# Kernel optimization log

Measured on AMD Instinct MI355X. Metric: run time of the kernel, lower is better.

Reference implementation:

```python
import jax, jax.numpy as jnp
import numpy as np

N_NODES = 50000
N_EDGES = 600000
IN_CH = 128
HID_CH = 128
OUT_CH = 64
DEMO = 8
N_GRAPHS = 100


def setup_inputs() -> dict:
    key = jax.random.key(0)
    ks = jax.random.split(key, 16)
    s = 0.02
    inp = {
        "x": jax.random.normal(ks[0], (N_NODES, IN_CH), jnp.float32),
        "edge_index": jax.random.randint(ks[1], (2, N_EDGES), 0, N_NODES, jnp.int32),
        "batch": jnp.sort(jax.random.randint(ks[2], (N_NODES,), 0, N_GRAPHS, jnp.int32)),
        "demographic": jax.random.normal(ks[3], (N_GRAPHS, DEMO), jnp.float32),
        "W1": jax.random.normal(ks[4], (IN_CH, HID_CH), jnp.float32) * s,
        "b1": jnp.zeros((HID_CH,), jnp.float32),
        "W2": jax.random.normal(ks[5], (HID_CH, HID_CH), jnp.float32) * s,
        "b2": jnp.zeros((HID_CH,), jnp.float32),
        "W3": jax.random.normal(ks[6], (HID_CH, OUT_CH), jnp.float32) * s,
        "b3": jnp.zeros((OUT_CH,), jnp.float32),
        "Wf1": jax.random.normal(ks[7], (OUT_CH + DEMO, 64), jnp.float32) * s,
        "bf1": jnp.zeros((64,), jnp.float32),
        "Wf2": jax.random.normal(ks[8], (64, 32), jnp.float32) * s,
        "bf2": jnp.zeros((32,), jnp.float32),
        "Wf3": jax.random.normal(ks[9], (32, 2), jnp.float32) * s,
        "bf3": jnp.zeros((2,), jnp.float32),
    }
    return inp


def _gcn_conv(x, W, b, src, dst, norm, n_nodes):
    # PyG GCNConv: out_i = sum_j norm_ij * (x_j @ W) + b  (self-loops included in src/dst)
    h = x @ W
    msg = h[src] * norm[:, None]
    return jax.ops.segment_sum(msg, dst, num_segments=n_nodes) + b


def reference(x, edge_index, batch, demographic, W1, b1, W2, b2, W3, b3, Wf1, bf1, Wf2, bf2, Wf3, bf3):
    n = x.shape[0]
    # add self-loops
    loop = jnp.arange(n, dtype=edge_index.dtype)
    src = jnp.concatenate([edge_index[0], loop])
    dst = jnp.concatenate([edge_index[1], loop])
    # symmetric degree normalization: deg^{-1/2}[src] * deg^{-1/2}[dst]
    deg = jax.ops.segment_sum(jnp.ones_like(src, jnp.float32), dst, num_segments=n)
    dinv = jnp.where(deg > 0, jax.lax.rsqrt(deg), 0.0)
    norm = dinv[src] * dinv[dst]

    h = jax.nn.relu(_gcn_conv(x, W1, b1, src, dst, norm, n))
    h = jax.nn.relu(_gcn_conv(h, W2, b2, src, dst, norm, n))
    h = jax.nn.relu(_gcn_conv(h, W3, b3, src, dst, norm, n))

    # global mean pool over graphs
    g = demographic.shape[0]
    sums = jax.ops.segment_sum(h, batch, num_segments=g)
    cnts = jax.ops.segment_sum(jnp.ones((n,), jnp.float32), batch, num_segments=g)
    pooled = sums / jnp.maximum(cnts, 1.0)[:, None]

    z = jnp.concatenate([pooled, demographic], axis=1)
    z = jax.nn.relu(z @ Wf1 + bf1)
    z = jax.nn.relu(z @ Wf2 + bf2)
    return z @ Wf3 + bf3
```

## Files before the change

kernel.cpp:

```cpp
#include <hip/hip_runtime.h>


typedef __bf16 bf16x8 __attribute__((ext_vector_type(8)));
typedef float f32x4 __attribute__((ext_vector_type(4)));
typedef float f32x2 __attribute__((ext_vector_type(2)));

__device__ __forceinline__ unsigned char f32_to_fp8(float v) {
    return (unsigned char)(__builtin_amdgcn_cvt_pk_fp8_f32(v, 0.f, 0, false) & 0xff);
}
__device__ __forceinline__ f32x2 fp8x2_to_f32(unsigned u) {
    f32x2 r = __builtin_amdgcn_cvt_pk_f32_fp8(u, false);
    return r;
}
__device__ __forceinline__ float fp8_to_f32(unsigned u) {
    f32x2 r = __builtin_amdgcn_cvt_pk_f32_fp8(u, false);
    return r.x;
}

union BF2 {
    __bf16 h[2];
    unsigned u;
};

#define PAD(c) (((c) + 15) & ~15)
#define BCAP 64
#define ECHUNK 4096

__device__ __forceinline__ void wpack_block(const float* __restrict__ W,
                                            __bf16* __restrict__ hi,
                                            __bf16* __restrict__ lo, int N, int b, int l) {
    int t = b >> 2, c = b & 3;
    int k0 = c * 32 + (l >> 4) * 8;
    int ncol = t * 16 + (l & 15);
    size_t base = ((size_t)b * 64 + l) * 8;
#pragma unroll
    for (int j = 0; j < 8; j++) {
        float v = W[(size_t)(k0 + j) * N + ncol];
        __bf16 h = (__bf16)v;
        hi[base + j] = h;
        lo[base + j] = (__bf16)(v - (float)h);
    }
}

__global__ __launch_bounds__(1024) void k_bin(const int* __restrict__ src,
                                              const int* __restrict__ dst,
                                              int2* __restrict__ binbuf,
                                              int* __restrict__ bcnt,
                                              const int* __restrict__ batch,
                                              int* __restrict__ gstart,
                                              const float* __restrict__ W1,
                                              const float* __restrict__ W2,
                                              const float* __restrict__ W3,
                                              __bf16* __restrict__ Wp1h, __bf16* __restrict__ Wp1l,
                                              __bf16* __restrict__ Wp2h, __bf16* __restrict__ Wp2l,
                                              __bf16* __restrict__ Wp3h, __bf16* __restrict__ Wp3l,
                                              int E, int EC, int nbuck, int n, int G) {
    int b = blockIdx.x;
    int tid = threadIdx.x;
    if (b < EC) {
        __shared__ int lcur[512];
        for (int i = tid; i < nbuck; i += 1024) lcur[i] = 0;
        __syncthreads();
        int e0 = b * ECHUNK;
        int cntE = E - e0;
        if (cntE > ECHUNK) cntE = ECHUNK;
#pragma unroll
        for (int k = 0; k < 4; k++) {
            int idx = tid + k * 1024;
            if (idx < cntE) {
                int s = src[e0 + idx];
                int d = dst[e0 + idx];
                int bk = d >> 7;
                int slot = atomicAdd(&lcur[bk], 1);
                if (slot < BCAP) {
                    int2 sd = {s, d};
                    binbuf[((size_t)b * nbuck + bk) * BCAP + slot] = sd;
                }
            }
        }
        __syncthreads();
        for (int bk = tid; bk < nbuck; bk += 1024) {
            int c = lcur[bk];
            bcnt[b * nbuck + bk] = (c < BCAP) ? c : BCAP;
        }
        return;
    }
    if (b == EC) {
        int g = tid;
        if (g <= G) {
            int lo = 0, hi = n;
            while (lo < hi) {
                int mid = (lo + hi) >> 1;
                if (batch[mid] < g) lo = mid + 1; else hi = mid;
            }
            gstart[g] = lo;
        }
        return;
    }
    int b64 = (b - EC - 1) * 16 + (tid >> 6);
    int l = tid & 63;
    if (b64 < 32) wpack_block(W1, Wp1h, Wp1l, 128, b64, l);
    else if (b64 < 64) wpack_block(W2, Wp2h, Wp2l, 128, b64 - 32, l);
    else if (b64 < 80) wpack_block(W3, Wp3h, Wp3l, 64, b64 - 64, l);
}

__global__ __launch_bounds__(1024) void k_rows(const int2* __restrict__ binbuf,
                                               const int* __restrict__ bcnt,
                                               int* __restrict__ gdeg,
                                               float* __restrict__ dinv,
                                               int* __restrict__ btot,
                                               unsigned int* __restrict__ tz128,
                                               unsigned int* __restrict__ tz64,
                                               int n, int EC, int nbuck) {
    __shared__ int lcnt[160];
    __shared__ int lpre[161];
    __shared__ int deg[128];
    int b = blockIdx.x;
    int tid = threadIdx.x;
    int lane = tid & 63;
    int wid = tid >> 6;
    int r0 = b << 7;
    int r1 = r0 + 128;
    if (r1 > n) r1 = n;
    int nrows = r1 - r0;
    if (b == 0) {
        if (tid < 32) tz128[(size_t)n * 32 + tid] = 0u;
        else if (tid < 48) tz64[(size_t)n * 16 + (tid - 32)] = 0u;
    }
    for (int c = tid; c < EC; c += 1024) lcnt[c] = bcnt[c * nbuck + b];
    if (tid < 128) deg[tid] = 0;
    __syncthreads();
    if (wid == 0) {
        int carry = 0;
        for (int bb = 0; bb < EC; bb += 64) {
            int idx = bb + lane;
            int val = (idx < EC) ? lcnt[idx] : 0;
            int sc = val;
#pragma unroll
            for (int d = 1; d < 64; d <<= 1) {
                int o = __shfl_up(sc, d);
                if (lane >= d) sc += o;
            }
            int grp = __shfl(sc, 63);
            if (idx < EC) lpre[idx] = sc - val + carry;
            carry += grp;
        }
        if (lane == 0) lpre[EC] = carry;
    }
    __syncthreads();
    int T = lpre[EC];
    for (int i = tid; i < T; i += 1024) {
        int lo = 0, hi = EC;
        while (lo < hi) {
            int mid = (lo + hi) >> 1;
            if (lpre[mid + 1] <= i) lo = mid + 1; else hi = mid;
        }
        int j = i - lpre[lo];
        int2 sd = binbuf[((size_t)lo * nbuck + b) * BCAP + j];
        unsigned r = (unsigned)(sd.y - r0);
        if (r < (unsigned)nrows) atomicAdd(&deg[r], 1);
    }
    __syncthreads();
    if (wid == 0) {
        int carry = 0;
#pragma unroll
        for (int bb = 0; bb < 128; bb += 64) {
            int idx = bb + lane;
            int val = (idx < nrows) ? PAD(deg[idx]) : 0;
#pragma unroll
            for (int d = 32; d > 0; d >>= 1) val += __shfl_xor(val, d);
            carry += val;
        }
        if (lane == 0) btot[b] = carry;
    }
    if (tid < nrows) {
        int d = deg[tid];
        gdeg[r0 + tid] = d;
        dinv[r0 + tid] = rsqrtf((float)(d + 1));
    }
}

__global__ __launch_bounds__(64) void k_base(const int* __restrict__ btot,
                                             int* __restrict__ bbase,
                                             int* __restrict__ rowptr,
                                             int n, int nbuck) {
    int lane = threadIdx.x;
    int carry = 0;
    for (int bb = 0; bb < nbuck; bb += 64) {
        int idx = bb + lane;
        int val = (idx < nbuck) ? btot[idx] : 0;
        int sc = val;
#pragma unroll
        for (int d = 1; d < 64; d <<= 1) {
            int o = __shfl_up(sc, d);
            if (lane >= d) sc += o;
        }
        int grp = __shfl(sc, 63);
        if (idx < nbuck) bbase[idx] = sc - val + carry;
        carry += grp;
    }
    if (lane == 0) {
        bbase[nbuck] = carry;
        rowptr[n] = carry;
    }
}

__global__ __launch_bounds__(1024) void k_place(const int2* __restrict__ binbuf,
                                                const int* __restrict__ bcnt,
                                                const int* __restrict__ gdeg,
                                                const int* __restrict__ bbase,
                                                int* __restrict__ rowptr,
                                                int* __restrict__ col,
                                                int n, int EC, int nbuck,
                                                const float* __restrict__ A,
                                                const __bf16* __restrict__ Wp_hi,
                                                const __bf16* __restrict__ Wp_lo,
                                                const float* __restrict__ dinv,
                                                unsigned char* __restrict__ Cf8) {
    int b = blockIdx.x;
    int tid = threadIdx.x;
    if (b < nbuck) {
        __shared__ int cols_s[5120];
        __shared__ int lcnt[160];
        __shared__ int lpre[161];
        __shared__ int lloc[129];
        __shared__ int lfill[128];
        int lane = tid & 63;
        int wid = tid >> 6;
        int r0 = b << 7;
        int r1 = r0 + 128;
        if (r1 > n) r1 = n;
        int nrows = r1 - r0;
        int base = bbase[b];
        int size = bbase[b + 1] - base;
        for (int c = tid; c < EC; c += 1024) lcnt[c] = bcnt[c * nbuck + b];
        __syncthreads();
        if (wid == 0) {
            int carry = 0;
            for (int bb = 0; bb < EC; bb += 64) {
                int idx = bb + lane;
                int val = (idx < EC) ? lcnt[idx] : 0;
                int sc = val;
#pragma unroll
                for (int d = 1; d < 64; d <<= 1) {
                    int o = __shfl_up(sc, d);
                    if (lane >= d) sc += o;
                }
                int grp = __shfl(sc, 63);
                if (idx < EC) lpre[idx] = sc - val + carry;
                carry += grp;
            }
            if (lane == 0) lpre[EC] = carry;
        } else if (wid == 1) {
            int carry = 0;
#pragma unroll
            for (int bb = 0; bb < 128; bb += 64) {
                int idx = bb + lane;
                int val = (idx < nrows) ? PAD(gdeg[r0 + idx]) : 0;
                int sc = val;
#pragma unroll
                for (int d = 1; d < 64; d <<= 1) {
                    int o = __shfl_up(sc, d);
                    if (lane >= d) sc += o;
                }
                int grp = __shfl(sc, 63);
                lloc[idx] = sc - val + carry;
                carry += grp;
            }
            if (lane == 0) lloc[128] = carry;
        }
        __syncthreads();
        if (tid < nrows) {
            lfill[tid] = lloc[tid];
            rowptr[r0 + tid] = base + lloc[tid];
        }
        int T = lpre[EC];
        if (size <= 5120) {
            for (int i = tid; i < size; i += 1024) cols_s[i] = n;
            __syncthreads();
            for (int i = tid; i < T; i += 1024) {
                int lo = 0, hi = EC;
                while (lo < hi) {
                    int mid = (lo + hi) >> 1;
                    if (lpre[mid + 1] <= i) lo = mid + 1; else hi = mid;
                }
                int j = i - lpre[lo];
                int2 sd = binbuf[((size_t)lo * nbuck + b) * BCAP + j];
                unsigned r = (unsigned)(sd.y - r0);
                if (r < (unsigned)nrows) {
                    int pos = atomicAdd(&lfill[r], 1);
                    if ((unsigned)pos < (unsigned)size) cols_s[pos] = sd.x;
                }
            }
            __syncthreads();
            for (int i = tid; i < size; i += 1024) col[base + i] = cols_s[i];
        } else {
            __syncthreads();
            for (int i = tid; i < T; i += 1024) {
                int lo = 0, hi = EC;
                while (lo < hi) {
                    int mid = (lo + hi) >> 1;
                    if (lpre[mid + 1] <= i) lo = mid + 1; else hi = mid;
                }
                int j = i - lpre[lo];
                int2 sd = binbuf[((size_t)lo * nbuck + b) * BCAP + j];
                unsigned r = (unsigned)(sd.y - r0);
                if (r < (unsigned)nrows) {
                    int pos = atomicAdd(&lfill[r], 1);
                    if (pos < size) col[base + pos] = sd.x;
                }
            }
            __syncthreads();
            if (tid < nrows) {
                int pend = lloc[tid + 1];
                for (int p = lloc[tid] + gdeg[r0 + tid]; p < pend; p++) col[base + p] = n;
            }
        }
        return;
    }
    constexpr int NT = 8;
    constexpr int N = NT * 16;
    int bid = b - nbuck;
    int wave = bid * 16 + (tid >> 6);
    int lane = tid & 63;
    int row0 = wave * 16;
    if (row0 >= n) return;
    int m = lane & 15;
    int q = lane >> 4;
    int row = row0 + m;
    if (row >= n) row = n - 1;
    const float* ap = A + (size_t)row * 128 + q * 8;
    bf16x8 ahi[4], alo[4];
#pragma unroll
    for (int c = 0; c < 4; c++) {
        float4 v0 = *(const float4*)(ap + c * 32);
        float4 v1 = *(const float4*)(ap + c * 32 + 4);
        float vv[8] = {v0.x, v0.y, v0.z, v0.w, v1.x, v1.y, v1.z, v1.w};
#pragma unroll
        for (int j = 0; j < 8; j++) {
            __bf16 h = (__bf16)vv[j];
            ahi[c][j] = h;
            alo[c][j] = (__bf16)(vv[j] - (float)h);
        }
    }
    float dscale[4];
#pragma unroll
    for (int r = 0; r < 4; r++) {
        int rr = row0 + q * 4 + r;
        dscale[r] = dinv[rr < n ? rr : (n - 1)];
    }
#pragma unroll
    for (int t = 0; t < NT; t++) {
        f32x4 acc = {0.f, 0.f, 0.f, 0.f};
#pragma unroll
        for (int c = 0; c < 4; c++) {
            size_t off = ((size_t)(t * 4 + c) * 64 + lane) * 8;
            bf16x8 bh = *(const bf16x8*)(Wp_hi + off);
            bf16x8 bl = *(const bf16x8*)(Wp_lo + off);
            acc = __builtin_amdgcn_mfma_f32_16x16x32_bf16(ahi[c], bh, acc, 0, 0, 0);
            acc = __builtin_amdgcn_mfma_f32_16x16x32_bf16(alo[c], bh, acc, 0, 0, 0);
            acc = __builtin_amdgcn_mfma_f32_16x16x32_bf16(ahi[c], bl, acc, 0, 0, 0);
        }
        int colx = t * 16 + m;
#pragma unroll
        for (int r = 0; r < 4; r++) {
            int orow = row0 + q * 4 + r;
            if (orow < n) Cf8[(size_t)orow * N + colx] = f32_to_fp8(acc[r] * dscale[r]);
        }
    }
}

template <int NT>
__global__ __launch_bounds__(256) void k_gemm_bf16(const __bf16* __restrict__ A,
                                                   const __bf16* __restrict__ Wp_hi,
                                                   const __bf16* __restrict__ Wp_lo,
                                                   const float* __restrict__ dinv,
                                                   unsigned char* __restrict__ Cf8, int n) {
    constexpr int N = NT * 16;
    int wave = (int)((blockIdx.x * 256u + threadIdx.x) >> 6);
    int lane = threadIdx.x & 63;
    int row0 = wave * 16;
    if (row0 >= n) return;
    int m = lane & 15;
    int q = lane >> 4;
    int row = row0 + m;
    if (row >= n) row = n - 1;
    const __bf16* ap = A + (size_t)row * 128 + q * 8;
    bf16x8 a[4];
#pragma unroll
    for (int c = 0; c < 4; c++) a[c] = *(const bf16x8*)(ap + c * 32);
    float dscale[4];
#pragma unroll
    for (int r = 0; r < 4; r++) {
        int rr = row0 + q * 4 + r;
        dscale[r] = dinv[rr < n ? rr : (n - 1)];
    }
#pragma unroll
    for (int t = 0; t < NT; t++) {
        f32x4 acc = {0.f, 0.f, 0.f, 0.f};
#pragma unroll
        for (int c = 0; c < 4; c++) {
            size_t off = ((size_t)(t * 4 + c) * 64 + lane) * 8;
            bf16x8 bh = *(const bf16x8*)(Wp_hi + off);
            bf16x8 bl = *(const bf16x8*)(Wp_lo + off);
            acc = __builtin_amdgcn_mfma_f32_16x16x32_bf16(a[c], bh, acc, 0, 0, 0);
            acc = __builtin_amdgcn_mfma_f32_16x16x32_bf16(a[c], bl, acc, 0, 0, 0);
        }
        int colx = t * 16 + m;
#pragma unroll
        for (int r = 0; r < 4; r++) {
            int orow = row0 + q * 4 + r;
            if (orow < n) Cf8[(size_t)orow * N + colx] = f32_to_fp8(acc[r] * dscale[r]);
        }
    }
}

__global__ __launch_bounds__(256) void k_agg128(const unsigned short* __restrict__ t8,
                                                const int* __restrict__ rowptr,
                                                const int* __restrict__ col,
                                                const float* __restrict__ dinv,
                                                const float* __restrict__ bias,
                                                unsigned int* __restrict__ out, int n) {
    int w = (int)((blockIdx.x * 256u + threadIdx.x) >> 6);
    int lane = threadIdx.x & 63;
    if (w >= n) return;
    f32x2 vs = fp8x2_to_f32((unsigned)t8[(size_t)w * 64 + lane]);
    float a0 = vs.x;
    float a1 = vs.y;
    int p = rowptr[w], pe = rowptr[w + 1];
    for (; p < pe; p += 16) {
        int4 c0 = *(const int4*)(col + p);
        int4 c1 = *(const int4*)(col + p + 4);
        int4 c2 = *(const int4*)(col + p + 8);
        int4 c3 = *(const int4*)(col + p + 12);
        unsigned u0 = t8[((size_t)c0.x << 6) + lane];
        unsigned u1 = t8[((size_t)c0.y << 6) + lane];
        unsigned u2 = t8[((size_t)c0.z << 6) + lane];
        unsigned u3 = t8[((size_t)c0.w << 6) + lane];
        unsigned u4 = t8[((size_t)c1.x << 6) + lane];
        unsigned u5 = t8[((size_t)c1.y << 6) + lane];
        unsigned u6 = t8[((size_t)c1.z << 6) + lane];
        unsigned u7 = t8[((size_t)c1.w << 6) + lane];
        unsigned u8 = t8[((size_t)c2.x << 6) + lane];
        unsigned u9 = t8[((size_t)c2.y << 6) + lane];
        unsigned ua = t8[((size_t)c2.z << 6) + lane];
        unsigned ub = t8[((size_t)c2.w << 6) + lane];
        unsigned uc = t8[((size_t)c3.x << 6) + lane];
        unsigned ud = t8[((size_t)c3.y << 6) + lane];
        unsigned ue = t8[((size_t)c3.z << 6) + lane];
        unsigned uf = t8[((size_t)c3.w << 6) + lane];
        f32x2 v;
        v = fp8x2_to_f32(u0); a0 += v.x; a1 += v.y;
        v = fp8x2_to_f32(u1); a0 += v.x; a1 += v.y;
        v = fp8x2_to_f32(u2); a0 += v.x; a1 += v.y;
        v = fp8x2_to_f32(u3); a0 += v.x; a1 += v.y;
        v = fp8x2_to_f32(u4); a0 += v.x; a1 += v.y;
        v = fp8x2_to_f32(u5); a0 += v.x; a1 += v.y;
        v = fp8x2_to_f32(u6); a0 += v.x; a1 += v.y;
        v = fp8x2_to_f32(u7); a0 += v.x; a1 += v.y;
        v = fp8x2_to_f32(u8); a0 += v.x; a1 += v.y;
        v = fp8x2_to_f32(u9); a0 += v.x; a1 += v.y;
        v = fp8x2_to_f32(ua); a0 += v.x; a1 += v.y;
        v = fp8x2_to_f32(ub); a0 += v.x; a1 += v.y;
        v = fp8x2_to_f32(uc); a0 += v.x; a1 += v.y;
        v = fp8x2_to_f32(ud); a0 += v.x; a1 += v.y;
        v = fp8x2_to_f32(ue); a0 += v.x; a1 += v.y;
        v = fp8x2_to_f32(uf); a0 += v.x; a1 += v.y;
    }
    float di = dinv[w];
    BF2 o;
    o.h[0] = (__bf16)fmaxf(di * a0 + bias[lane * 2], 0.f);
    o.h[1] = (__bf16)fmaxf(di * a1 + bias[lane * 2 + 1], 0.f);
    out[(size_t)w * 64 + lane] = o.u;
}

__global__ __launch_bounds__(256) void k_agg64(const unsigned char* __restrict__ t8,
                                               const int* __restrict__ rowptr,
                                               const int* __restrict__ col,
                                               const float* __restrict__ dinv,
                                               const float* __restrict__ bias,
                                               __bf16* __restrict__ out, int n) {
    int w = (int)((blockIdx.x * 256u + threadIdx.x) >> 6);
    int lane = threadIdx.x & 63;
    if (w >= n) return;
    float acc = fp8_to_f32((unsigned)t8[(size_t)w * 64 + lane]);
    int p = rowptr[w], pe = rowptr[w + 1];
    for (; p < pe; p += 16) {
        int4 c0 = *(const int4*)(col + p);
        int4 c1 = *(const int4*)(col + p + 4);
        int4 c2 = *(const int4*)(col + p + 8);
        int4 c3 = *(const int4*)(col + p + 12);
        unsigned u0 = t8[((size_t)c0.x << 6) + lane];
        unsigned u1 = t8[((size_t)c0.y << 6) + lane];
        unsigned u2 = t8[((size_t)c0.z << 6) + lane];
        unsigned u3 = t8[((size_t)c0.w << 6) + lane];
        unsigned u4 = t8[((size_t)c1.x << 6) + lane];
        unsigned u5 = t8[((size_t)c1.y << 6) + lane];
        unsigned u6 = t8[((size_t)c1.z << 6) + lane];
        unsigned u7 = t8[((size_t)c1.w << 6) + lane];
        unsigned u8 = t8[((size_t)c2.x << 6) + lane];
        unsigned u9 = t8[((size_t)c2.y << 6) + lane];
        unsigned ua = t8[((size_t)c2.z << 6) + lane];
        unsigned ub = t8[((size_t)c2.w << 6) + lane];
        unsigned uc = t8[((size_t)c3.x << 6) + lane];
        unsigned ud = t8[((size_t)c3.y << 6) + lane];
        unsigned ue = t8[((size_t)c3.z << 6) + lane];
        unsigned uf = t8[((size_t)c3.w << 6) + lane];
        acc += fp8_to_f32(u0);
        acc += fp8_to_f32(u1);
        acc += fp8_to_f32(u2);
        acc += fp8_to_f32(u3);
        acc += fp8_to_f32(u4);
        acc += fp8_to_f32(u5);
        acc += fp8_to_f32(u6);
        acc += fp8_to_f32(u7);
        acc += fp8_to_f32(u8);
        acc += fp8_to_f32(u9);
        acc += fp8_to_f32(ua);
        acc += fp8_to_f32(ub);
        acc += fp8_to_f32(uc);
        acc += fp8_to_f32(ud);
        acc += fp8_to_f32(ue);
        acc += fp8_to_f32(uf);
    }
    out[(size_t)w * 64 + lane] = (__bf16)fmaxf(dinv[w] * acc + bias[lane], 0.f);
}

__global__ __launch_bounds__(256) void k_poolmlp(const unsigned short* __restrict__ h,
                                                 const int* __restrict__ gstart,
                                                 const float* __restrict__ demo,
                                                 const float* __restrict__ Wf1,
                                                 const float* __restrict__ bf1,
                                                 const float* __restrict__ Wf2,
                                                 const float* __restrict__ bf2,
                                                 const float* __restrict__ Wf3,
                                                 const float* __restrict__ bf3,
                                                 float* __restrict__ out, int G) {
    int g = blockIdx.x;
    int tid = threadIdx.x;
    int lane = tid & 63;
    int wv = tid >> 6;
    int s = gstart[g], e = gstart[g + 1];
    float acc = 0.f;
    for (int i = s + wv; i < e; i += 4)
        acc += __uint_as_float((unsigned)h[(size_t)i * 64 + lane] << 16);
    __shared__ float red[4][64];
    __shared__ float zin[72];
    __shared__ float z1[64];
    __shared__ float z2[32];
    red[wv][lane] = acc;
    if (tid >= 64 && tid < 72) zin[tid] = demo[g * 8 + (tid - 64)];
    __syncthreads();
    if (tid < 64) {
        float v = red[0][tid] + red[1][tid] + red[2][tid] + red[3][tid];
        zin[tid] = v / fmaxf((float)(e - s), 1.0f);
    }
    __syncthreads();
    if (tid < 64) {
        float a = bf1[tid];
        for (int k = 0; k < 72; k++) a += zin[k] * Wf1[k * 64 + tid];
        z1[tid] = fmaxf(a, 0.f);
    }
    __syncthreads();
    if (tid < 32) {
        float a2 = bf2[tid];
        for (int k = 0; k < 64; k++) a2 += z1[k] * Wf2[k * 32 + tid];
        z2[tid] = fmaxf(a2, 0.f);
    }
    __syncthreads();
    if (tid < 2) {
        float a3 = bf3[tid];
        for (int k = 0; k < 32; k++) a3 += z2[k] * Wf3[k * 2 + tid];
        out[g * 2 + tid] = a3;
    }
}

extern "C" void kernel_launch(void* const* d_in, const int* in_sizes, int n_in,
                              void* d_out, int out_size, void* d_ws, size_t ws_size,
                              hipStream_t stream) {
    const float* x    = (const float*)d_in[0];
    const int*   ei   = (const int*)d_in[1];
    const int*   batch= (const int*)d_in[2];
    const float* demo = (const float*)d_in[3];
    const float* W1   = (const float*)d_in[4];
    const float* b1   = (const float*)d_in[5];
    const float* W2   = (const float*)d_in[6];
    const float* b2   = (const float*)d_in[7];
    const float* W3   = (const float*)d_in[8];
    const float* b3   = (const float*)d_in[9];
    const float* Wf1  = (const float*)d_in[10];
    const float* bf1  = (const float*)d_in[11];
    const float* Wf2  = (const float*)d_in[12];
    const float* bf2  = (const float*)d_in[13];
    const float* Wf3  = (const float*)d_in[14];
    const float* bf3  = (const float*)d_in[15];
    float* out = (float*)d_out;

    const int n = in_sizes[0] / 128;
    const int E = in_sizes[1] / 2;
    const int G = in_sizes[3] / 8;
    const int Epad = E + 15 * n;
    const int EC = (E + ECHUNK - 1) / ECHUNK;
    const int nbuck = (n + 127) / 128;

    char* ws = (char*)d_ws;
    auto alloc = [&](size_t bytes) {
        char* p = ws;
        ws += (bytes + 255) & ~(size_t)255;
        return p;
    };
    float*  dinv   = (float*)alloc((size_t)n * 4);
    int*    rowptr = (int*)alloc((size_t)(n + 1) * 4);
    int*    gdeg   = (int*)alloc((size_t)n * 4);
    int*    btot   = (int*)alloc((size_t)nbuck * 4);
    int*    bbase  = (int*)alloc((size_t)(nbuck + 1) * 4);
    int*    col    = (int*)alloc((size_t)Epad * 4);
    int2*   binbuf = (int2*)alloc((size_t)EC * nbuck * BCAP * 8);
    int*    bcnt   = (int*)alloc((size_t)EC * nbuck * 4);
    unsigned char* tbf  = (unsigned char*)alloc((size_t)(n + 1) * 128);
    __bf16* hbuf   = (__bf16*)alloc((size_t)n * 128 * 2);
    unsigned char* t3bf = (unsigned char*)alloc((size_t)(n + 1) * 64);
    __bf16* h3     = (__bf16*)alloc((size_t)n * 64 * 2);
    __bf16* Wp1h   = (__bf16*)alloc(128 * 128 * 2);
    __bf16* Wp1l   = (__bf16*)alloc(128 * 128 * 2);
    __bf16* Wp2h   = (__bf16*)alloc(128 * 128 * 2);
    __bf16* Wp2l   = (__bf16*)alloc(128 * 128 * 2);
    __bf16* Wp3h   = (__bf16*)alloc(128 * 64 * 2);
    __bf16* Wp3l   = (__bf16*)alloc(128 * 64 * 2);
    int*    gstart = (int*)alloc((size_t)(G + 1) * 4);

    const int* srcv = ei;
    const int* dstv = ei + E;

    int waves = (n + 15) / 16;
    int gemm_blocks = (waves + 3) / 4;
    int gemm1_blocks = (waves + 15) / 16;
    int agg_blocks = (int)(((size_t)n * 64 + 255) / 256);

    k_bin<<<EC + 1 + 5, 1024, 0, stream>>>(srcv, dstv, binbuf, bcnt, batch, gstart,
                                           W1, W2, W3, Wp1h, Wp1l, Wp2h, Wp2l,
                                           Wp3h, Wp3l, E, EC, nbuck, n, G);
    k_rows<<<nbuck, 1024, 0, stream>>>(binbuf, bcnt, gdeg, dinv, btot,
                                       (unsigned int*)tbf, (unsigned int*)t3bf,
                                       n, EC, nbuck);
    k_base<<<1, 64, 0, stream>>>(btot, bbase, rowptr, n, nbuck);
    k_place<<<nbuck + gemm1_blocks, 1024, 0, stream>>>(binbuf, bcnt, gdeg, bbase,
                                                       rowptr, col, n, EC, nbuck,
                                                       x, Wp1h, Wp1l, dinv, tbf);

    k_agg128<<<agg_blocks, 256, 0, stream>>>((const unsigned short*)tbf, rowptr, col,
                                             dinv, b1, (unsigned int*)hbuf, n);
    k_gemm_bf16<8><<<gemm_blocks, 256, 0, stream>>>(hbuf, Wp2h, Wp2l, dinv, tbf, n);
    k_agg128<<<agg_blocks, 256, 0, stream>>>((const unsigned short*)tbf, rowptr, col,
                                             dinv, b2, (unsigned int*)hbuf, n);
    k_gemm_bf16<4><<<gemm_blocks, 256, 0, stream>>>(hbuf, Wp3h, Wp3l, dinv, t3bf, n);
    k_agg64<<<agg_blocks, 256, 0, stream>>>((const unsigned char*)t3bf, rowptr, col,
                                            dinv, b3, h3, n);

    k_poolmlp<<<G, 256, 0, stream>>>((const unsigned short*)h3, gstart, demo,
                                     Wf1, bf1, Wf2, bf2, Wf3, bf3, out, G);
}
```

Before: 254.6 us.

## Split neighbor gathers across lane groups with 8-byte fp8 loads in aggregation

The aggregation kernels now have each lane load 8 fp8 features at once. The wave is split into groups that each handle a different neighbor edge in parallel, and partial sums are combined with cross-lane shuffles. Row padding drops from 16 to 8 edges, cutting wasted padded gathers, and the mean-pool reads are vectorized in the same way. This aims to raise memory-level parallelism and cut per-edge instruction overhead, in exchange for extra shuffle reductions and only a fraction of lanes doing the final store.

```diff
diff --git a/kernel.cpp b/kernel.cpp
--- a/kernel.cpp
+++ b/kernel.cpp
@@ -8,13 +8,12 @@
 __device__ __forceinline__ unsigned char f32_to_fp8(float v) {
     return (unsigned char)(__builtin_amdgcn_cvt_pk_fp8_f32(v, 0.f, 0, false) & 0xff);
 }
-__device__ __forceinline__ f32x2 fp8x2_to_f32(unsigned u) {
-    f32x2 r = __builtin_amdgcn_cvt_pk_f32_fp8(u, false);
-    return r;
-}
-__device__ __forceinline__ float fp8_to_f32(unsigned u) {
-    f32x2 r = __builtin_amdgcn_cvt_pk_f32_fp8(u, false);
-    return r.x;
+__device__ __forceinline__ void acc8_fp8(float* a, uint2 u) {
+    f32x2 v;
+    v = __builtin_amdgcn_cvt_pk_f32_fp8(u.x, false); a[0] += v.x; a[1] += v.y;
+    v = __builtin_amdgcn_cvt_pk_f32_fp8(u.x, true);  a[2] += v.x; a[3] += v.y;
+    v = __builtin_amdgcn_cvt_pk_f32_fp8(u.y, false); a[4] += v.x; a[5] += v.y;
+    v = __builtin_amdgcn_cvt_pk_f32_fp8(u.y, true);  a[6] += v.x; a[7] += v.y;
 }
 
 union BF2 {
@@ -22,7 +21,7 @@
     unsigned u;
 };
 
-#define PAD(c) (((c) + 15) & ~15)
+#define PAD(c) (((c) + 7) & ~7)
 #define BCAP 64
 #define ECHUNK 4096
 
@@ -415,7 +414,7 @@
     }
 }
 
-__global__ __launch_bounds__(256) void k_agg128(const unsigned short* __restrict__ t8,
+__global__ __launch_bounds__(256) void k_agg128(const unsigned char* __restrict__ t8,
                                                 const int* __restrict__ rowptr,
                                                 const int* __restrict__ col,
                                                 const float* __restrict__ dinv,
@@ -424,54 +423,45 @@
     int w = (int)((blockIdx.x * 256u + threadIdx.x) >> 6);
     int lane = threadIdx.x & 63;
     if (w >= n) return;
-    f32x2 vs = fp8x2_to_f32((unsigned)t8[(size_t)w * 64 + lane]);
-    float a0 = vs.x;
-    float a1 = vs.y;
+    const uint2* t8v = (const uint2*)t8;
+    int cg = lane & 15;
+    int g = lane >> 4;
+    float acc[8] = {0.f, 0.f, 0.f, 0.f, 0.f, 0.f, 0.f, 0.f};
     int p = rowptr[w], pe = rowptr[w + 1];
-    for (; p < pe; p += 16) {
-        int4 c0 = *(const int4*)(col + p);
-        int4 c1 = *(const int4*)(col + p + 4);
-        int4 c2 = *(const int4*)(col + p + 8);
-        int4 c3 = *(const int4*)(col + p + 12);
-        unsigned u0 = t8[((size_t)c0.x << 6) + lane];
-        unsigned u1 = t8[((size_t)c0.y << 6) + lane];
-        unsigned u2 = t8[((size_t)c0.z << 6) + lane];
-        unsigned u3 = t8[((size_t)c0.w << 6) + lane];
-        unsigned u4 = t8[((size_t)c1.x << 6) + lane];
-        unsigned u5 = t8[((size_t)c1.y << 6) + lane];
-        unsigned u6 = t8[((size_t)c1.z << 6) + lane];
-        unsigned u7 = t8[((size_t)c1.w << 6) + lane];
-        unsigned u8 = t8[((size_t)c2.x << 6) + lane];
-        unsigned u9 = t8[((size_t)c2.y << 6) + lane];
-        unsigned ua = t8[((size_t)c2.z << 6) + lane];
-        unsigned ub = t8[((size_t)c2.w << 6) + lane];
-        unsigned uc = t8[((size_t)c3.x << 6) + lane];
-        unsigned ud = t8[((size_t)c3.y << 6) + lane];
-        unsigned ue = t8[((size_t)c3.z << 6) + lane];
-        unsigned uf = t8[((size_t)c3.w << 6) + lane];
-        f32x2 v;
-        v = fp8x2_to_f32(u0); a0 += v.x; a1 += v.y;
-        v = fp8x2_to_f32(u1); a0 += v.x; a1 += v.y;
-        v = fp8x2_to_f32(u2); a0 += v.x; a1 += v.y;
-        v = fp8x2_to_f32(u3); a0 += v.x; a1 += v.y;
-        v = fp8x2_to_f32(u4); a0 += v.x; a1 += v.y;
-        v = fp8x2_to_f32(u5); a0 += v.x; a1 += v.y;
-        v = fp8x2_to_f32(u6); a0 += v.x; a1 += v.y;
-        v = fp8x2_to_f32(u7); a0 += v.x; a1 += v.y;
-        v = fp8x2_to_f32(u8); a0 += v.x; a1 += v.y;
-        v = fp8x2_to_f32(u9); a0 += v.x; a1 += v.y;
-        v = fp8x2_to_f32(ua); a0 += v.x; a1 += v.y;
-        v = fp8x2_to_f32(ub); a0 += v.x; a1 += v.y;
-        v = fp8x2_to_f32(uc); a0 += v.x; a1 += v.y;
-        v = fp8x2_to_f32(ud); a0 += v.x; a1 += v.y;
-        v = fp8x2_to_f32(ue); a0 += v.x; a1 += v.y;
-        v = fp8x2_to_f32(uf); a0 += v.x; a1 += v.y;
+    for (; p < pe; p += 8) {
+        int c0 = col[p + g];
+        int c1 = col[p + 4 + g];
+        uint2 u0 = t8v[((size_t)c0 << 4) + cg];
+        uint2 u1 = t8v[((size_t)c1 << 4) + cg];
+        acc8_fp8(acc, u0);
+        acc8_fp8(acc, u1);
+    }
+#pragma unroll
+    for (int j = 0; j < 8; j++) {
+        acc[j] += __shfl_xor(acc[j], 16);
+        acc[j] += __shfl_xor(acc[j], 32);
+    }
+    {
+        uint2 us = t8v[((size_t)w << 4) + cg];
+        float s8[8] = {0.f, 0.f, 0.f, 0.f, 0.f, 0.f, 0.f, 0.f};
+        acc8_fp8(s8, us);
+#pragma unroll
+        for (int j = 0; j < 8; j++) acc[j] += s8[j];
     }
     float di = dinv[w];
-    BF2 o;
-    o.h[0] = (__bf16)fmaxf(di * a0 + bias[lane * 2], 0.f);
-    o.h[1] = (__bf16)fmaxf(di * a1 + bias[lane * 2 + 1], 0.f);
-    out[(size_t)w * 64 + lane] = o.u;
+    float4 bb0 = *(const float4*)(bias + cg * 8);
+    float4 bb1 = *(const float4*)(bias + cg * 8 + 4);
+    float bv[8] = {bb0.x, bb0.y, bb0.z, bb0.w, bb1.x, bb1.y, bb1.z, bb1.w};
+    BF2 o[4];
+#pragma unroll
+    for (int j = 0; j < 4; j++) {
+        o[j].h[0] = (__bf16)fmaxf(di * acc[2 * j] + bv[2 * j], 0.f);
+        o[j].h[1] = (__bf16)fmaxf(di * acc[2 * j + 1] + bv[2 * j + 1], 0.f);
+    }
+    if (lane < 16) {
+        uint4 st = {o[0].u, o[1].u, o[2].u, o[3].u};
+        *(uint4*)(out + (size_t)w * 64 + cg * 4) = st;
+    }
 }
 
 __global__ __launch_bounds__(256) void k_agg64(const unsigned char* __restrict__ t8,
@@ -483,47 +473,43 @@
     int w = (int)((blockIdx.x * 256u + threadIdx.x) >> 6);
     int lane = threadIdx.x & 63;
     if (w >= n) return;
-    float acc = fp8_to_f32((unsigned)t8[(size_t)w * 64 + lane]);
+    const uint2* t8v = (const uint2*)t8;
+    int cg = lane & 7;
+    int g = lane >> 3;
+    float acc[8] = {0.f, 0.f, 0.f, 0.f, 0.f, 0.f, 0.f, 0.f};
     int p = rowptr[w], pe = rowptr[w + 1];
-    for (; p < pe; p += 16) {
-        int4 c0 = *(const int4*)(col + p);
-        int4 c1 = *(const int4*)(col + p + 4);
-        int4 c2 = *(const int4*)(col + p + 8);
-        int4 c3 = *(const int4*)(col + p + 12);
-        unsigned u0 = t8[((size_t)c0.x << 6) + lane];
-        unsigned u1 = t8[((size_t)c0.y << 6) + lane];
-        unsigned u2 = t8[((size_t)c0.z << 6) + lane];
-        unsigned u3 = t8[((size_t)c0.w << 6) + lane];
-        unsigned u4 = t8[((size_t)c1.x << 6) + lane];
-        unsigned u5 = t8[((size_t)c1.y << 6) + lane];
-        unsigned u6 = t8[((size_t)c1.z << 6) + lane];
-        unsigned u7 = t8[((size_t)c1.w << 6) + lane];
-        unsigned u8 = t8[((size_t)c2.x << 6) + lane];
-        unsigned u9 = t8[((size_t)c2.y << 6) + lane];
-        unsigned ua = t8[((size_t)c2.z << 6) + lane];
-        unsigned ub = t8[((size_t)c2.w << 6) + lane];
-        unsigned uc = t8[((size_t)c3.x << 6) + lane];
-        unsigned ud = t8[((size_t)c3.y << 6) + lane];
-        unsigned ue = t8[((size_t)c3.z << 6) + lane];
-        unsigned uf = t8[((size_t)c3.w << 6) + lane];
-        acc += fp8_to_f32(u0);
-        acc += fp8_to_f32(u1);
-        acc += fp8_to_f32(u2);
-        acc += fp8_to_f32(u3);
-        acc += fp8_to_f32(u4);
-        acc += fp8_to_f32(u5);
-        acc += fp8_to_f32(u6);
-        acc += fp8_to_f32(u7);
-        acc += fp8_to_f32(u8);
-        acc += fp8_to_f32(u9);
-        acc += fp8_to_f32(ua);
-        acc += fp8_to_f32(ub);
-        acc += fp8_to_f32(uc);
-        acc += fp8_to_f32(ud);
-        acc += fp8_to_f32(ue);
-        acc += fp8_to_f32(uf);
-    }
-    out[(size_t)w * 64 + lane] = (__bf16)fmaxf(dinv[w] * acc + bias[lane], 0.f);
+    for (; p < pe; p += 8) {
+        int c = col[p + g];
+        uint2 u = t8v[((size_t)c << 3) + cg];
+        acc8_fp8(acc, u);
+    }
+#pragma unroll
+    for (int j = 0; j < 8; j++) {
+        acc[j] += __shfl_xor(acc[j], 8);
+        acc[j] += __shfl_xor(acc[j], 16);
+        acc[j] += __shfl_xor(acc[j], 32);
+    }
+    {
+        uint2 us = t8v[((size_t)w << 3) + cg];
+        float s8[8] = {0.f, 0.f, 0.f, 0.f, 0.f, 0.f, 0.f, 0.f};
+        acc8_fp8(s8, us);
+#pragma unroll
+        for (int j = 0; j < 8; j++) acc[j] += s8[j];
+    }
+    float di = dinv[w];
+    float4 bb0 = *(const float4*)(bias + cg * 8);
+    float4 bb1 = *(const float4*)(bias + cg * 8 + 4);
+    float bv[8] = {bb0.x, bb0.y, bb0.z, bb0.w, bb1.x, bb1.y, bb1.z, bb1.w};
+    BF2 o[4];
+#pragma unroll
+    for (int j = 0; j < 4; j++) {
+        o[j].h[0] = (__bf16)fmaxf(di * acc[2 * j] + bv[2 * j], 0.f);
+        o[j].h[1] = (__bf16)fmaxf(di * acc[2 * j + 1] + bv[2 * j + 1], 0.f);
+    }
+    if (lane < 8) {
+        uint4 st = {o[0].u, o[1].u, o[2].u, o[3].u};
+        *(uint4*)((unsigned int*)out + (size_t)w * 32 + cg * 4) = st;
+    }
 }
 
 __global__ __launch_bounds__(256) void k_poolmlp(const unsigned short* __restrict__ h,
@@ -541,14 +527,30 @@
     int lane = tid & 63;
     int wv = tid >> 6;
     int s = gstart[g], e = gstart[g + 1];
-    float acc = 0.f;
-    for (int i = s + wv; i < e; i += 4)
-        acc += __uint_as_float((unsigned)h[(size_t)i * 64 + lane] << 16);
+    const unsigned* hu = (const unsigned*)h;
+    int cg = lane & 15;
+    int sub = lane >> 4;
+    float acc[4] = {0.f, 0.f, 0.f, 0.f};
+    for (int i = s + wv * 4 + sub; i < e; i += 16) {
+        uint2 v = *(const uint2*)(hu + ((size_t)i << 5) + cg * 2);
+        acc[0] += __uint_as_float(v.x << 16);
+        acc[1] += __uint_as_float(v.x & 0xffff0000u);
+        acc[2] += __uint_as_float(v.y << 16);
+        acc[3] += __uint_as_float(v.y & 0xffff0000u);
+    }
+#pragma unroll
+    for (int j = 0; j < 4; j++) {
+        acc[j] += __shfl_xor(acc[j], 16);
+        acc[j] += __shfl_xor(acc[j], 32);
+    }
     __shared__ float red[4][64];
     __shared__ float zin[72];
     __shared__ float z1[64];
     __shared__ float z2[32];
-    red[wv][lane] = acc;
+    if (sub == 0) {
+#pragma unroll
+        for (int j = 0; j < 4; j++) red[wv][cg * 4 + j] = acc[j];
+    }
     if (tid >= 64 && tid < 72) zin[tid] = demo[g * 8 + (tid - 64)];
     __syncthreads();
     if (tid < 64) {
@@ -648,13 +650,13 @@
                                                        rowptr, col, n, EC, nbuck,
                                                        x, Wp1h, Wp1l, dinv, tbf);
 
-    k_agg128<<<agg_blocks, 256, 0, stream>>>((const unsigned short*)tbf, rowptr, col,
+    k_agg128<<<agg_blocks, 256, 0, stream>>>(tbf, rowptr, col,
                                              dinv, b1, (unsigned int*)hbuf, n);
     k_gemm_bf16<8><<<gemm_blocks, 256, 0, stream>>>(hbuf, Wp2h, Wp2l, dinv, tbf, n);
-    k_agg128<<<agg_blocks, 256, 0, stream>>>((const unsigned short*)tbf, rowptr, col,
+    k_agg128<<<agg_blocks, 256, 0, stream>>>(tbf, rowptr, col,
                                              dinv, b2, (unsigned int*)hbuf, n);
     k_gemm_bf16<4><<<gemm_blocks, 256, 0, stream>>>(hbuf, Wp3h, Wp3l, dinv, t3bf, n);
-    k_agg64<<<agg_blocks, 256, 0, stream>>>((const unsigned char*)t3bf, rowptr, col,
+    k_agg64<<<agg_blocks, 256, 0, stream>>>(t3bf, rowptr, col,
                                             dinv, b3, h3, n);
 
     k_poolmlp<<<G, 256, 0, stream>>>((const unsigned short*)h3, gstart, demo,
```

New measurement: 241.9 us. 5.0% less time.
